# Performance work log

Hardware: AMD Instinct MI355X
Metric: run time of the kernel (lower is better)

Reference implementation:

```python
import jax, jax.numpy as jnp
import numpy as np

N = 20000   # nodes
E = 320000  # edges
F0 = 32     # num_features
H = 8       # GAT heads
G = 64      # graphs in batch


def setup_inputs() -> dict:
    key = jax.random.key(0)
    ks = jax.random.split(key, 16)
    def p(k, shape, s=0.05):
        return jax.random.normal(k, shape, jnp.float32) * s
    d = {}
    d['x'] = jax.random.normal(ks[0], (N, F0), jnp.float32)
    d['edge_index'] = jax.random.randint(ks[1], (2, E), 0, N, dtype=jnp.int32)
    d['edge_weights'] = jax.random.uniform(ks[2], (E,), jnp.float32)
    d['batch'] = jnp.sort(jax.random.randint(ks[3], (N,), 0, G, dtype=jnp.int32))
    # GATConv(32 -> 32, heads=8)
    d['W_gat'] = p(ks[4], (F0, H * F0)); d['att_src'] = p(ks[5], (H, F0))
    d['att_dst'] = p(ks[6], (H, F0));    d['b_gat'] = jnp.zeros((H * F0,), jnp.float32)
    # residual Linear(256 -> 1024) (widened so the residual add is shape-consistent)
    d['W_res'] = p(ks[7], (H * F0, 1024)); d['b_res'] = jnp.zeros((1024,), jnp.float32)
    # GCNConv(256 -> 512) + BN1
    d['W2'] = p(ks[8], (H * F0, 512)); d['b2'] = jnp.zeros((512,), jnp.float32)
    d['g1'] = jnp.ones((512,), jnp.float32); d['be1'] = jnp.zeros((512,), jnp.float32)
    d['m1'] = jnp.zeros((512,), jnp.float32); d['v1'] = jnp.ones((512,), jnp.float32)
    # GCNConv(512 -> 1024) + BN2
    d['W3'] = p(ks[9], (512, 1024)); d['b3'] = jnp.zeros((1024,), jnp.float32)
    d['g2'] = jnp.ones((1024,), jnp.float32); d['be2'] = jnp.zeros((1024,), jnp.float32)
    d['m2'] = jnp.zeros((1024,), jnp.float32); d['v2'] = jnp.ones((1024,), jnp.float32)
    # head
    d['Wf1'] = p(ks[10], (1024, 256)); d['bf1'] = jnp.zeros((256,), jnp.float32)
    d['Wf2'] = p(ks[11], (256, 2));    d['bf2'] = jnp.zeros((2,), jnp.float32)
    return d


def _add_self_loops(edge_index, edge_weight, n):
    loop = jnp.arange(n, dtype=edge_index.dtype)
    ei = jnp.concatenate([edge_index, jnp.stack([loop, loop])], axis=1)
    ew = jnp.concatenate([edge_weight, jnp.ones((n,), edge_weight.dtype)])
    return ei, ew


def _gat(x, edge_index, W, att_src, att_dst, b, n):
    # PyG GATConv, concat=True, eval (attention dropout off). Self-loops already added.
    src, dst = edge_index[0], edge_index[1]
    h = (x @ W).reshape(n, H, -1)                    # [N,H,C]
    a_s = jnp.einsum('nhc,hc->nh', h, att_src)        # [N,H]
    a_d = jnp.einsum('nhc,hc->nh', h, att_dst)
    e = jax.nn.leaky_relu(a_s[src] + a_d[dst], 0.2)   # [E,H]
    m = jax.ops.segment_max(e, dst, num_segments=n)   # softmax over incoming edges
    ex = jnp.exp(e - m[dst])
    s = jax.ops.segment_sum(ex, dst, num_segments=n)
    alpha = ex / s[dst]
    out = jax.ops.segment_sum(h[src] * alpha[:, :, None], dst, num_segments=n)
    return out.reshape(n, -1) + b                     # [N,H*C]


def _gcn(x, edge_index, w, W, b, n):
    # PyG GCNConv with symmetric normalization; self-loops (weight 1) already added.
    src, dst = edge_index[0], edge_index[1]
    deg = jax.ops.segment_sum(w, dst, num_segments=n)
    dinv = jnp.where(deg > 0, jax.lax.rsqrt(jnp.maximum(deg, 1e-12)), 0.0)
    norm = dinv[src] * w * dinv[dst]                  # [E]
    h = x @ W                                         # transform first (cheaper)
    return jax.ops.segment_sum(h[src] * norm[:, None], dst, num_segments=n) + b


def _bn(x, g, b, m, v):
    return g * (x - m) * jax.lax.rsqrt(v + 1e-5) + b


def reference(x, edge_index, edge_weights, batch, W_gat, att_src, att_dst, b_gat,
              W_res, b_res, W2, b2, g1, be1, m1, v1, W3, b3, g2, be2, m2, v2,
              Wf1, bf1, Wf2, bf2):
    n = x.shape[0]
    ei, ew = _add_self_loops(edge_index, edge_weights, n)
    h = jax.nn.relu(_gat(x, ei, W_gat, att_src, att_dst, b_gat, n))   # [N,256]
    res = h @ W_res + b_res                                           # [N,1024]
    h = _gcn(h, ei, ew, W2, b2, n)                                    # [N,512]
    h = jax.nn.relu(_bn(h, g1, be1, m1, v1))
    h = _gcn(h, ei, ew, W3, b3, n)                                    # [N,1024]
    h = jax.nn.relu(_bn(h, g2, be2, m2, v2))
    h = h + res
    pooled = jax.ops.segment_max(h, batch, num_segments=G)            # global max pool [G,1024]
    z = jax.nn.relu(pooled @ Wf1 + bf1)                               # dropout is eval no-op
    return z @ Wf2 + bf2                                              # [G,2]
```

## Files before the change

### kernel.cpp

```cpp
#include <hip/hip_runtime.h>
#include <hip/hip_bf16.h>

#define NN 20000
#define EE 320000
#define GG 64
#define EN (EE + NN)
#define MT 157

typedef float f32x4 __attribute__((ext_vector_type(4)));
typedef __bf16 bf16x4 __attribute__((ext_vector_type(4)));
typedef __bf16 bf16x8 __attribute__((ext_vector_type(8)));

__device__ __forceinline__ void gl_lds16(const void* g, void* l) {
    __builtin_amdgcn_global_load_lds((const __attribute__((address_space(1))) void*)g,
                                     (__attribute__((address_space(3))) void*)l, 16, 0, 0);
}

__global__ void sentinel_kernel(float* out, int n) {
    int i = blockIdx.x * 256 + threadIdx.x;
    if (i < n) out[i] = 12345.0f;
}

__global__ void init_kernel(int* deg_cnt, float* deg_w, int* fill, float* pooled) {
    int i = blockIdx.x * 256 + threadIdx.x;
    if (i < NN) { deg_cnt[i] = 1; deg_w[i] = 1.0f; fill[i] = 0; }
    if (i < GG * 1024) pooled[i] = -INFINITY;
}

__global__ void convert_wt(const float* __restrict__ W, __bf16* __restrict__ Wt, int K, int N) {
    int n = blockIdx.x;
    for (int k = threadIdx.x; k < K; k += 256)
        Wt[(size_t)n * K + k] = (__bf16)W[(size_t)k * N + n];
}

__global__ __launch_bounds__(256) void gat_transform(
    const float* __restrict__ x, const float* __restrict__ W,
    const float* __restrict__ att_s, const float* __restrict__ att_d,
    __bf16* __restrict__ hlin, float* __restrict__ a_s, float* __restrict__ a_d)
{
    __shared__ float Ws[32 * 256];
    int tid = threadIdx.x;
#pragma unroll
    for (int k = 0; k < 32; k++) Ws[k * 256 + tid] = W[k * 256 + tid];
    float asc = att_s[tid], adc = att_d[tid];
    __syncthreads();
    for (int n = blockIdx.x; n < NN; n += gridDim.x) {
        const float* xp = x + (size_t)n * 32;
        float acc = 0.f;
#pragma unroll
        for (int k = 0; k < 32; k++) acc += xp[k] * Ws[k * 256 + tid];
        hlin[(size_t)n * 256 + tid] = (__bf16)acc;
        float s = acc * asc, d = acc * adc;
#pragma unroll
        for (int m = 1; m <= 16; m <<= 1) { s += __shfl_xor(s, m); d += __shfl_xor(d, m); }
        if ((tid & 31) == 0) { int h = tid >> 5; a_s[n * 8 + h] = s; a_d[n * 8 + h] = d; }
    }
}

__global__ void deg_kernel(const int* __restrict__ ei, const float* __restrict__ ew,
                           int* deg_cnt, float* deg_w) {
    int e = blockIdx.x * 256 + threadIdx.x;
    if (e >= EE) return;
    int dst = ei[EE + e];
    atomicAdd(&deg_cnt[dst], 1);
    atomicAdd(&deg_w[dst], ew[e]);
}

__global__ __launch_bounds__(256) void scan_kernel(const int* __restrict__ deg_cnt, int* __restrict__ rowptr) {
    __shared__ int partial[256];
    int tid = threadIdx.x;
    const int chunk = (NN + 255) / 256;
    int s0 = tid * chunk, s1 = min(s0 + chunk, NN);
    int sum = 0;
    for (int i = s0; i < s1; i++) sum += deg_cnt[i];
    partial[tid] = sum;
    __syncthreads();
    if (tid == 0) {
        int run = 0;
        for (int i = 0; i < 256; i++) { int t = partial[i]; partial[i] = run; run += t; }
        rowptr[NN] = run;
    }
    __syncthreads();
    int run = partial[tid];
    for (int i = s0; i < s1; i++) { rowptr[i] = run; run += deg_cnt[i]; }
}

__global__ void fill_kernel(const int* __restrict__ ei, const float* __restrict__ ew,
                            const float* __restrict__ deg_w, const int* __restrict__ rowptr,
                            int* fill, int* __restrict__ csr_src, float* __restrict__ csr_norm) {
    int e = blockIdx.x * 256 + threadIdx.x;
    if (e >= EN) return;
    int src, dst; float w;
    if (e < EE) { src = ei[e]; dst = ei[EE + e]; w = ew[e]; }
    else        { src = dst = e - EE; w = 1.0f; }
    int pos = atomicAdd(&fill[dst], 1);
    int slot = rowptr[dst] + pos;
    csr_src[slot] = src;
    csr_norm[slot] = rsqrtf(deg_w[src]) * w * rsqrtf(deg_w[dst]);
}

__global__ __launch_bounds__(256) void gat_agg(
    const int* __restrict__ rowptr, const int* __restrict__ csr_src,
    const float* __restrict__ a_s, const float* __restrict__ a_d,
    const __bf16* __restrict__ hlin, const float* __restrict__ b_gat,
    __bf16* __restrict__ h1)
{
    int widx = threadIdx.x >> 6, lane = threadIdx.x & 63;
    int node = blockIdx.x * 4 + widx;
    int base = rowptr[node], deg = rowptr[node + 1] - base;
    int hA = lane & 7;
    int eslot = lane >> 3;
    int hB = lane >> 3;
    float adA = a_d[node * 8 + hA];
    float acc[4] = {0.f, 0.f, 0.f, 0.f};

    if (deg <= 64) {
        int sv = (lane < deg) ? csr_src[base + lane] : 0;
        float ev[8];
        float psum = 0.f;
#pragma unroll
        for (int j = 0; j < 8; j++) {
            int e = j * 8 + eslot;
            float v = 0.f;
            if (e < deg) {
                int src = __shfl(sv, e);
                float t = a_s[src * 8 + hA] + adA;
                t = (t > 0.f) ? t : 0.2f * t;
                v = __expf(t);
            }
            ev[j] = v;
            psum += v;
        }
#pragma unroll
        for (int m = 8; m <= 32; m <<= 1) psum += __shfl_xor(psum, m);
        float sinv = 1.f / __shfl(psum, hB);
#pragma unroll
        for (int j = 0; j < 8; j++) {
            if (j * 8 >= deg) break;
            int lim = min(8, deg - j * 8);
            for (int t = 0; t < lim; t++) {
                int s = j * 8 + t;
                int src = __shfl(sv, s);
                float alpha = __shfl(ev[j], (t << 3) | hB) * sinv;
                bf16x4 f = *(const bf16x4*)(hlin + (size_t)src * 256 + lane * 4);
#pragma unroll
                for (int c = 0; c < 4; c++) acc[c] += alpha * (float)f[c];
            }
        }
    } else {
        float sum = 0.f;
        for (int e = 0; e < deg; e++) {
            int src = csr_src[base + e];
            float t = a_s[src * 8 + hA] + adA;
            t = (t > 0.f) ? t : 0.2f * t;
            sum += __expf(t);
        }
        float sinv = 1.f / __shfl(sum, hB);
        float adB = a_d[node * 8 + hB];
        for (int e = 0; e < deg; e++) {
            int src = csr_src[base + e];
            float t = a_s[src * 8 + hB] + adB;
            t = (t > 0.f) ? t : 0.2f * t;
            float alpha = __expf(t) * sinv;
            bf16x4 f = *(const bf16x4*)(hlin + (size_t)src * 256 + lane * 4);
#pragma unroll
            for (int c = 0; c < 4; c++) acc[c] += alpha * (float)f[c];
        }
    }
    float4 bg = *(const float4*)(b_gat + lane * 4);
    bf16x4 o;
    o[0] = (__bf16)fmaxf(acc[0] + bg.x, 0.f);
    o[1] = (__bf16)fmaxf(acc[1] + bg.y, 0.f);
    o[2] = (__bf16)fmaxf(acc[2] + bg.z, 0.f);
    o[3] = (__bf16)fmaxf(acc[3] + bg.w, 0.f);
    *(bf16x4*)(h1 + (size_t)node * 256 + lane * 4) = o;
}

template <int C>
__global__ __launch_bounds__(256) void gcn_agg(
    const int* __restrict__ rowptr, const int* __restrict__ csr_src,
    const float* __restrict__ csr_norm, const __bf16* __restrict__ feat,
    __bf16* __restrict__ out)
{
    constexpr int V = C / 64;
    int widx = threadIdx.x >> 6, lane = threadIdx.x & 63;
    int node = blockIdx.x * 4 + widx;
    int base = rowptr[node], deg = rowptr[node + 1] - base;
    float acc[V];
#pragma unroll
    for (int j = 0; j < V; j++) acc[j] = 0.f;
    const __bf16* fb = feat + lane * V;
    for (int e0 = 0; e0 < deg; e0 += 64) {
        int cnt = min(64, deg - e0);
        int sv = 0; float wv = 0.f;
        if (lane < cnt) { sv = csr_src[base + e0 + lane]; wv = csr_norm[base + e0 + lane]; }
#pragma unroll 4
        for (int s = 0; s < cnt; s++) {
            int src = __shfl(sv, s);
            float w = __shfl(wv, s);
            if constexpr (V == 8) {
                bf16x8 f = *(const bf16x8*)(fb + (size_t)src * C);
#pragma unroll
                for (int j = 0; j < 8; j++) acc[j] += w * (float)f[j];
            } else {
                bf16x4 f = *(const bf16x4*)(fb + (size_t)src * C);
#pragma unroll
                for (int j = 0; j < 4; j++) acc[j] += w * (float)f[j];
            }
        }
    }
    if constexpr (V == 8) {
        bf16x8 o;
#pragma unroll
        for (int j = 0; j < 8; j++) o[j] = (__bf16)acc[j];
        *(bf16x8*)(out + (size_t)node * C + lane * V) = o;
    } else {
        bf16x4 o;
#pragma unroll
        for (int j = 0; j < 4; j++) o[j] = (__bf16)acc[j];
        *(bf16x4*)(out + (size_t)node * C + lane * V) = o;
    }
}


__device__ __forceinline__ void stage_async(
    const __bf16* __restrict__ A, int K, const __bf16* __restrict__ Wt,
    int bm, int bn, int k0, int tid, __bf16* As, __bf16* Bs)
{
#pragma unroll
    for (int i = 0; i < 2; i++) {
        int j = i * 256 + tid;
        int r = j >> 2, c = j & 3;
        const __bf16* gp = A + (size_t)(bm + r) * K + k0 + c * 8;
        gl_lds16(gp, As + (size_t)(j & ~63) * 8);
    }
#pragma unroll
    for (int i = 0; i < 2; i++) {
        int j = i * 256 + tid;
        int r = j >> 2, c = j & 3;
        const __bf16* gp = Wt + (size_t)(bn + r) * K + k0 + c * 8;
        gl_lds16(gp, Bs + (size_t)(j & ~63) * 8);
    }
}

__device__ __forceinline__ void mfma_step(
    const __bf16* As, const __bf16* Bs, int wr, int wc, int l16, int q, f32x4 (&acc)[4][4])
{
    bf16x8 af[4], bfv[4];
#pragma unroll
    for (int mt = 0; mt < 4; mt++) af[mt]  = *(const bf16x8*)(As + (wr * 64 + mt * 16 + l16) * 32 + q * 8);
#pragma unroll
    for (int nt = 0; nt < 4; nt++) bfv[nt] = *(const bf16x8*)(Bs + (wc * 64 + nt * 16 + l16) * 32 + q * 8);
#pragma unroll
    for (int mt = 0; mt < 4; mt++)
#pragma unroll
        for (int nt = 0; nt < 4; nt++)
            acc[mt][nt] = __builtin_amdgcn_mfma_f32_16x16x32_bf16(af[mt], bfv[nt], acc[mt][nt], 0, 0, 0);
}

__device__ __forceinline__ void gemm_loop(
    const __bf16* __restrict__ A, int K, const __bf16* __restrict__ Wt,
    int bm, int bn, int tid, int wr, int wc, int l16, int q,
    __bf16* As, __bf16* Bs, f32x4 (&acc)[4][4])
{
    for (int k0 = 0; k0 < K; k0 += 32) {
        stage_async(A, K, Wt, bm, bn, k0, tid, As, Bs);
        __syncthreads();
        mfma_step(As, Bs, wr, wc, l16, q, acc);
        __syncthreads();
    }
}

__global__ __launch_bounds__(256) void gemm_bn_relu(
    const __bf16* __restrict__ A, const __bf16* __restrict__ Wt,
    int M, int K, int Nc,
    const float* __restrict__ bias,
    const float* __restrict__ g, const float* __restrict__ be,
    const float* __restrict__ mu, const float* __restrict__ var,
    __bf16* __restrict__ C)
{
    __shared__ __bf16 As[128 * 32];
    __shared__ __bf16 Bs[128 * 32];
    int tid = threadIdx.x;
    int w = tid >> 6, wr = w >> 1, wc = w & 1;
    int l = tid & 63, q = l >> 4, l16 = l & 15;
    int i = blockIdx.x;
    int k = (i & 3) * MT + (i >> 2);
    int bm = (k >> 2) * 128, bn = (k & 3) * 128;
    f32x4 acc[4][4] = {};
    gemm_loop(A, K, Wt, bm, bn, tid, wr, wc, l16, q, As, Bs, acc);
#pragma unroll
    for (int nt = 0; nt < 4; nt++) {
        int gn = bn + wc * 64 + nt * 16 + l16;
        float s = g[gn] * rsqrtf(var[gn] + 1e-5f);
        float t = be[gn] - mu[gn] * s;
        float bv = bias[gn];
#pragma unroll
        for (int mt = 0; mt < 4; mt++)
#pragma unroll
            for (int r = 0; r < 4; r++) {
                int gm = bm + wr * 64 + mt * 16 + q * 4 + r;
                if (gm < M) C[(size_t)gm * Nc + gn] = (__bf16)fmaxf((acc[mt][nt][r] + bv) * s + t, 0.f);
            }
    }
}

__device__ __forceinline__ void atomicMaxFloat(float* addr, float value) {
    if (value >= 0.f) atomicMax((int*)addr, __float_as_int(value));
    else              atomicMin((unsigned int*)addr, __float_as_uint(value));
}

__global__ __launch_bounds__(256) void gemm_final(
    const __bf16* __restrict__ A1, const __bf16* __restrict__ W3t,
    const __bf16* __restrict__ A2, const __bf16* __restrict__ Wrt,
    const float* __restrict__ b3, const float* __restrict__ bres,
    const float* __restrict__ g, const float* __restrict__ be,
    const float* __restrict__ mu, const float* __restrict__ var,
    const int* __restrict__ batch, float* __restrict__ pooled)
{
    const int M = NN;
    __shared__ __bf16 As[128 * 32];
    __shared__ __bf16 Bs[128 * 32];
    __shared__ int bat[128];
    int tid = threadIdx.x;
    int w = tid >> 6, wr = w >> 1, wc = w & 1;
    int l = tid & 63, q = l >> 4, l16 = l & 15;
    int i = blockIdx.x;
    int k = (i & 7) * MT + (i >> 3);
    int bm = (k >> 3) * 128, bn = (k & 7) * 128;
    if (tid < 128) bat[tid] = (bm + tid < M) ? batch[bm + tid] : -1;
    f32x4 acc[4][4] = {};
    f32x4 accR[4][4] = {};
    gemm_loop(A1, 512, W3t, bm, bn, tid, wr, wc, l16, q, As, Bs, acc);
    gemm_loop(A2, 256, Wrt, bm, bn, tid, wr, wc, l16, q, As, Bs, accR);
#pragma unroll
    for (int nt = 0; nt < 4; nt++) {
        int gn = bn + wc * 64 + nt * 16 + l16;
        float s = g[gn] * rsqrtf(var[gn] + 1e-5f);
        float t = be[gn] - mu[gn] * s;
        float bv3 = b3[gn];
        float bvr = bres[gn];
        int cb = -1; float run = 0.f;
#pragma unroll
        for (int mt = 0; mt < 4; mt++)
#pragma unroll
            for (int r = 0; r < 4; r++) {
                int lr = wr * 64 + mt * 16 + q * 4 + r;
                int id = bat[lr];
                if (id < 0) continue;
                float v = fmaxf((acc[mt][nt][r] + bv3) * s + t, 0.f) + accR[mt][nt][r] + bvr;
                if (id == cb) run = fmaxf(run, v);
                else {
                    if (cb >= 0) atomicMaxFloat(&pooled[cb * 1024 + gn], run);
                    cb = id; run = v;
                }
            }
        if (cb >= 0) atomicMaxFloat(&pooled[cb * 1024 + gn], run);
    }
}

__global__ __launch_bounds__(256) void head_kernel(
    const float* __restrict__ pooled, const float* __restrict__ Wf1, const float* __restrict__ bf1,
    const float* __restrict__ Wf2, const float* __restrict__ bf2, float* __restrict__ out)
{
    int gph = blockIdx.x, tid = threadIdx.x;
    __shared__ float prow[1024];
    __shared__ float zred[256];
    for (int i = tid; i < 1024; i += 256) prow[i] = pooled[gph * 1024 + i];
    __syncthreads();
    float z = 0.f;
    for (int k = 0; k < 1024; k++) z += prow[k] * Wf1[k * 256 + tid];
    z = fmaxf(z + bf1[tid], 0.f);
    for (int c = 0; c < 2; c++) {
        zred[tid] = z * Wf2[tid * 2 + c];
        __syncthreads();
        for (int s = 128; s > 0; s >>= 1) { if (tid < s) zred[tid] += zred[tid + s]; __syncthreads(); }
        if (tid == 0) out[gph * 2 + c] = zred[0] + bf2[c];
        __syncthreads();
    }
}

extern "C" void kernel_launch(void* const* d_in, const int* in_sizes, int n_in,
                              void* d_out, int out_size, void* d_ws, size_t ws_size,
                              hipStream_t stream) {
    const float* x       = (const float*)d_in[0];
    const int*   ei      = (const int*)d_in[1];
    const float* ew      = (const float*)d_in[2];
    const int*   batch   = (const int*)d_in[3];
    const float* W_gat   = (const float*)d_in[4];
    const float* att_src = (const float*)d_in[5];
    const float* att_dst = (const float*)d_in[6];
    const float* b_gat   = (const float*)d_in[7];
    const float* W_res   = (const float*)d_in[8];
    const float* b_res   = (const float*)d_in[9];
    const float* W2      = (const float*)d_in[10];
    const float* b2v     = (const float*)d_in[11];
    const float* g1      = (const float*)d_in[12];
    const float* be1     = (const float*)d_in[13];
    const float* m1      = (const float*)d_in[14];
    const float* v1      = (const float*)d_in[15];
    const float* W3      = (const float*)d_in[16];
    const float* b3      = (const float*)d_in[17];
    const float* g2      = (const float*)d_in[18];
    const float* be2     = (const float*)d_in[19];
    const float* m2      = (const float*)d_in[20];
    const float* v2      = (const float*)d_in[21];
    const float* Wf1     = (const float*)d_in[22];
    const float* bf1     = (const float*)d_in[23];
    const float* Wf2     = (const float*)d_in[24];
    const float* bf2v    = (const float*)d_in[25];
    float* out           = (float*)d_out;

    char* ws = (char*)d_ws;
    size_t off = 0;
    auto alloc = [&](size_t bytes) { size_t o = off; off += (bytes + 255) & ~(size_t)255; return o; };
    size_t o_hlin   = alloc((size_t)NN * 256 * 2);
    size_t o_h1     = alloc((size_t)NN * 256 * 2);
    size_t o_h2     = alloc((size_t)NN * 512 * 2);
    size_t o_agg2   = alloc((size_t)NN * 512 * 2);
    size_t o_as     = alloc((size_t)NN * 8 * 4);
    size_t o_ad     = alloc((size_t)NN * 8 * 4);
    size_t o_degc   = alloc((size_t)NN * 4);
    size_t o_degw   = alloc((size_t)NN * 4);
    size_t o_rowptr = alloc((size_t)(NN + 1) * 4);
    size_t o_fill   = alloc((size_t)NN * 4);
    size_t o_csrs   = alloc((size_t)EN * 4);
    size_t o_csrn   = alloc((size_t)EN * 4);
    size_t o_pool   = alloc((size_t)GG * 1024 * 4);
    size_t o_w2t    = alloc((size_t)512 * 256 * 2);
    size_t o_w3t    = alloc((size_t)1024 * 512 * 2);
    size_t o_wrt    = alloc((size_t)1024 * 256 * 2);
    if (off > ws_size) {
        sentinel_kernel<<<(out_size + 255) / 256, 256, 0, stream>>>(out, out_size);
        return;
    }

    __bf16* hlin   = (__bf16*)(ws + o_hlin);
    __bf16* agg1   = hlin;
    __bf16* h1     = (__bf16*)(ws + o_h1);
    __bf16* h2     = (__bf16*)(ws + o_h2);
    __bf16* agg2   = (__bf16*)(ws + o_agg2);
    float*  a_s    = (float*)(ws + o_as);
    float*  a_d    = (float*)(ws + o_ad);
    int*    degc   = (int*)(ws + o_degc);
    float*  degw   = (float*)(ws + o_degw);
    int*    rowptr = (int*)(ws + o_rowptr);
    int*    fillb  = (int*)(ws + o_fill);
    int*    csrs   = (int*)(ws + o_csrs);
    float*  csrn   = (float*)(ws + o_csrn);
    float*  pooled = (float*)(ws + o_pool);
    __bf16* W2t    = (__bf16*)(ws + o_w2t);
    __bf16* W3t    = (__bf16*)(ws + o_w3t);
    __bf16* Wrt    = (__bf16*)(ws + o_wrt);

    init_kernel<<<256, 256, 0, stream>>>(degc, degw, fillb, pooled);
    convert_wt<<<512, 256, 0, stream>>>(W2, W2t, 256, 512);
    convert_wt<<<1024, 256, 0, stream>>>(W3, W3t, 512, 1024);
    convert_wt<<<1024, 256, 0, stream>>>(W_res, Wrt, 256, 1024);

    gat_transform<<<512, 256, 0, stream>>>(x, W_gat, att_src, att_dst, hlin, a_s, a_d);
    deg_kernel<<<(EE + 255) / 256, 256, 0, stream>>>(ei, ew, degc, degw);
    scan_kernel<<<1, 256, 0, stream>>>(degc, rowptr);
    fill_kernel<<<(EN + 255) / 256, 256, 0, stream>>>(ei, ew, degw, rowptr, fillb, csrs, csrn);
    gat_agg<<<NN / 4, 256, 0, stream>>>(rowptr, csrs, a_s, a_d, hlin, b_gat, h1);

    gcn_agg<256><<<NN / 4, 256, 0, stream>>>(rowptr, csrs, csrn, h1, agg1);
    gemm_bn_relu<<<4 * MT, 256, 0, stream>>>(agg1, W2t, NN, 256, 512, b2v,
        g1, be1, m1, v1, h2);
    gcn_agg<512><<<NN / 4, 256, 0, stream>>>(rowptr, csrs, csrn, h2, agg2);
    gemm_final<<<8 * MT, 256, 0, stream>>>(agg2, W3t, h1, Wrt,
        b3, b_res, g2, be2, m2, v2, batch, pooled);

    head_kernel<<<GG, 256, 0, stream>>>(pooled, Wf1, bf1, Wf2, bf2v, out);
}
```

Baseline: 465.3 us.

## Double-buffer GEMM LDS staging and split aggregation accumulators for ILP

The GEMM main loop now uses two LDS buffers. The next K-slice is issued asynchronously while MFMAs run on the current one, and one barrier per step replaces two. The GAT and GCN gather loops process two edges per iteration into separate accumulators, so more independent loads are in flight. LDS use per block doubles, which may lower occupancy, and the extra accumulators raise register pressure.

Result: faster. 447.1 us (-3.9%).

```diff
diff --git a/kernel.cpp b/kernel.cpp
--- a/kernel.cpp
+++ b/kernel.cpp
@@ -112,7 +112,8 @@
     int eslot = lane >> 3;
     int hB = lane >> 3;
     float adA = a_d[node * 8 + hA];
-    float acc[4] = {0.f, 0.f, 0.f, 0.f};
+    float acc0[4] = {0.f, 0.f, 0.f, 0.f};
+    float acc1[4] = {0.f, 0.f, 0.f, 0.f};
 
     if (deg <= 64) {
         int sv = (lane < deg) ? csr_src[base + lane] : 0;
@@ -138,13 +139,24 @@
         for (int j = 0; j < 8; j++) {
             if (j * 8 >= deg) break;
             int lim = min(8, deg - j * 8);
-            for (int t = 0; t < lim; t++) {
-                int s = j * 8 + t;
-                int src = __shfl(sv, s);
+            int t = 0;
+            for (; t + 1 < lim; t += 2) {
+                int s0 = j * 8 + t, s1 = s0 + 1;
+                int srcA = __shfl(sv, s0), srcB = __shfl(sv, s1);
+                float aA = __shfl(ev[j], (t << 3) | hB) * sinv;
+                float aB = __shfl(ev[j], ((t + 1) << 3) | hB) * sinv;
+                bf16x4 fA = *(const bf16x4*)(hlin + (size_t)srcA * 256 + lane * 4);
+                bf16x4 fB = *(const bf16x4*)(hlin + (size_t)srcB * 256 + lane * 4);
+#pragma unroll
+                for (int c = 0; c < 4; c++) { acc0[c] += aA * (float)fA[c]; acc1[c] += aB * (float)fB[c]; }
+            }
+            if (t < lim) {
+                int s0 = j * 8 + t;
+                int src = __shfl(sv, s0);
                 float alpha = __shfl(ev[j], (t << 3) | hB) * sinv;
                 bf16x4 f = *(const bf16x4*)(hlin + (size_t)src * 256 + lane * 4);
 #pragma unroll
-                for (int c = 0; c < 4; c++) acc[c] += alpha * (float)f[c];
+                for (int c = 0; c < 4; c++) acc0[c] += alpha * (float)f[c];
             }
         }
     } else {
@@ -164,15 +176,15 @@
             float alpha = __expf(t) * sinv;
             bf16x4 f = *(const bf16x4*)(hlin + (size_t)src * 256 + lane * 4);
 #pragma unroll
-            for (int c = 0; c < 4; c++) acc[c] += alpha * (float)f[c];
+            for (int c = 0; c < 4; c++) acc0[c] += alpha * (float)f[c];
         }
     }
     float4 bg = *(const float4*)(b_gat + lane * 4);
     bf16x4 o;
-    o[0] = (__bf16)fmaxf(acc[0] + bg.x, 0.f);
-    o[1] = (__bf16)fmaxf(acc[1] + bg.y, 0.f);
-    o[2] = (__bf16)fmaxf(acc[2] + bg.z, 0.f);
-    o[3] = (__bf16)fmaxf(acc[3] + bg.w, 0.f);
+    o[0] = (__bf16)fmaxf(acc0[0] + acc1[0] + bg.x, 0.f);
+    o[1] = (__bf16)fmaxf(acc0[1] + acc1[1] + bg.y, 0.f);
+    o[2] = (__bf16)fmaxf(acc0[2] + acc1[2] + bg.z, 0.f);
+    o[3] = (__bf16)fmaxf(acc0[3] + acc1[3] + bg.w, 0.f);
     *(bf16x4*)(h1 + (size_t)node * 256 + lane * 4) = o;
 }
 
@@ -186,38 +198,54 @@
     int widx = threadIdx.x >> 6, lane = threadIdx.x & 63;
     int node = blockIdx.x * 4 + widx;
     int base = rowptr[node], deg = rowptr[node + 1] - base;
-    float acc[V];
-#pragma unroll
-    for (int j = 0; j < V; j++) acc[j] = 0.f;
+    float acc0[V], acc1[V];
+#pragma unroll
+    for (int j = 0; j < V; j++) { acc0[j] = 0.f; acc1[j] = 0.f; }
     const __bf16* fb = feat + lane * V;
     for (int e0 = 0; e0 < deg; e0 += 64) {
         int cnt = min(64, deg - e0);
         int sv = 0; float wv = 0.f;
         if (lane < cnt) { sv = csr_src[base + e0 + lane]; wv = csr_norm[base + e0 + lane]; }
-#pragma unroll 4
-        for (int s = 0; s < cnt; s++) {
+        int s = 0;
+#pragma unroll 2
+        for (; s + 1 < cnt; s += 2) {
+            int srcA = __shfl(sv, s),    srcB = __shfl(sv, s + 1);
+            float wA = __shfl(wv, s),    wB   = __shfl(wv, s + 1);
+            if constexpr (V == 8) {
+                bf16x8 fA = *(const bf16x8*)(fb + (size_t)srcA * C);
+                bf16x8 fB = *(const bf16x8*)(fb + (size_t)srcB * C);
+#pragma unroll
+                for (int j = 0; j < 8; j++) { acc0[j] += wA * (float)fA[j]; acc1[j] += wB * (float)fB[j]; }
+            } else {
+                bf16x4 fA = *(const bf16x4*)(fb + (size_t)srcA * C);
+                bf16x4 fB = *(const bf16x4*)(fb + (size_t)srcB * C);
+#pragma unroll
+                for (int j = 0; j < 4; j++) { acc0[j] += wA * (float)fA[j]; acc1[j] += wB * (float)fB[j]; }
+            }
+        }
+        if (s < cnt) {
             int src = __shfl(sv, s);
             float w = __shfl(wv, s);
             if constexpr (V == 8) {
                 bf16x8 f = *(const bf16x8*)(fb + (size_t)src * C);
 #pragma unroll
-                for (int j = 0; j < 8; j++) acc[j] += w * (float)f[j];
+                for (int j = 0; j < 8; j++) acc0[j] += w * (float)f[j];
             } else {
                 bf16x4 f = *(const bf16x4*)(fb + (size_t)src * C);
 #pragma unroll
-                for (int j = 0; j < 4; j++) acc[j] += w * (float)f[j];
+                for (int j = 0; j < 4; j++) acc0[j] += w * (float)f[j];
             }
         }
     }
     if constexpr (V == 8) {
         bf16x8 o;
 #pragma unroll
-        for (int j = 0; j < 8; j++) o[j] = (__bf16)acc[j];
+        for (int j = 0; j < 8; j++) o[j] = (__bf16)(acc0[j] + acc1[j]);
         *(bf16x8*)(out + (size_t)node * C + lane * V) = o;
     } else {
         bf16x4 o;
 #pragma unroll
-        for (int j = 0; j < 4; j++) o[j] = (__bf16)acc[j];
+        for (int j = 0; j < 4; j++) o[j] = (__bf16)(acc0[j] + acc1[j]);
         *(bf16x4*)(out + (size_t)node * C + lane * V) = o;
     }
 }
@@ -258,17 +286,22 @@
             acc[mt][nt] = __builtin_amdgcn_mfma_f32_16x16x32_bf16(af[mt], bfv[nt], acc[mt][nt], 0, 0, 0);
 }
 
-__device__ __forceinline__ void gemm_loop(
+__device__ __forceinline__ void gemm_loop_db(
     const __bf16* __restrict__ A, int K, const __bf16* __restrict__ Wt,
     int bm, int bn, int tid, int wr, int wc, int l16, int q,
-    __bf16* As, __bf16* Bs, f32x4 (&acc)[4][4])
-{
-    for (int k0 = 0; k0 < K; k0 += 32) {
-        stage_async(A, K, Wt, bm, bn, k0, tid, As, Bs);
+    __bf16* As0, __bf16* Bs0, __bf16* As1, __bf16* Bs1, f32x4 (&acc)[4][4])
+{
+    int nsteps = K >> 5;
+    stage_async(A, K, Wt, bm, bn, 0, tid, As0, Bs0);
+    for (int s = 0; s < nsteps; s++) {
+        __bf16* cA = (s & 1) ? As1 : As0;
+        __bf16* cB = (s & 1) ? Bs1 : Bs0;
         __syncthreads();
-        mfma_step(As, Bs, wr, wc, l16, q, acc);
-        __syncthreads();
-    }
+        if (s + 1 < nsteps)
+            stage_async(A, K, Wt, bm, bn, (s + 1) << 5, tid, (s & 1) ? As0 : As1, (s & 1) ? Bs0 : Bs1);
+        mfma_step(cA, cB, wr, wc, l16, q, acc);
+    }
+    __syncthreads();
 }
 
 __global__ __launch_bounds__(256) void gemm_bn_relu(
@@ -279,8 +312,7 @@
     const float* __restrict__ mu, const float* __restrict__ var,
     __bf16* __restrict__ C)
 {
-    __shared__ __bf16 As[128 * 32];
-    __shared__ __bf16 Bs[128 * 32];
+    __shared__ __bf16 As0[128 * 32], Bs0[128 * 32], As1[128 * 32], Bs1[128 * 32];
     int tid = threadIdx.x;
     int w = tid >> 6, wr = w >> 1, wc = w & 1;
     int l = tid & 63, q = l >> 4, l16 = l & 15;
@@ -288,7 +320,7 @@
     int k = (i & 3) * MT + (i >> 2);
     int bm = (k >> 2) * 128, bn = (k & 3) * 128;
     f32x4 acc[4][4] = {};
-    gemm_loop(A, K, Wt, bm, bn, tid, wr, wc, l16, q, As, Bs, acc);
+    gemm_loop_db(A, K, Wt, bm, bn, tid, wr, wc, l16, q, As0, Bs0, As1, Bs1, acc);
 #pragma unroll
     for (int nt = 0; nt < 4; nt++) {
         int gn = bn + wc * 64 + nt * 16 + l16;
@@ -319,8 +351,7 @@
     const int* __restrict__ batch, float* __restrict__ pooled)
 {
     const int M = NN;
-    __shared__ __bf16 As[128 * 32];
-    __shared__ __bf16 Bs[128 * 32];
+    __shared__ __bf16 As0[128 * 32], Bs0[128 * 32], As1[128 * 32], Bs1[128 * 32];
     __shared__ int bat[128];
     int tid = threadIdx.x;
     int w = tid >> 6, wr = w >> 1, wc = w & 1;
@@ -331,8 +362,8 @@
     if (tid < 128) bat[tid] = (bm + tid < M) ? batch[bm + tid] : -1;
     f32x4 acc[4][4] = {};
     f32x4 accR[4][4] = {};
-    gemm_loop(A1, 512, W3t, bm, bn, tid, wr, wc, l16, q, As, Bs, acc);
-    gemm_loop(A2, 256, Wrt, bm, bn, tid, wr, wc, l16, q, As, Bs, accR);
+    gemm_loop_db(A1, 512, W3t, bm, bn, tid, wr, wc, l16, q, As0, Bs0, As1, Bs1, acc);
+    gemm_loop_db(A2, 256, Wrt, bm, bn, tid, wr, wc, l16, q, As0, Bs0, As1, Bs1, accR);
 #pragma unroll
     for (int nt = 0; nt < 4; nt++) {
         int gn = bn + wc * 64 + nt * 16 + l16;
```

## Tile weight transpose through LDS and unroll gathers with independent accumulators

Applied to the files above, without the earlier changes.

Weight conversion now transposes 64x64 tiles through padded shared memory, so both the reads and the writes are coalesced instead of strided. The GAT and GCN aggregation loops now handle four edges per iteration, issuing four independent row gathers and accumulating into four separate register sets. This aims to raise memory-level parallelism on the random neighbour loads. It costs more registers, which may lower occupancy, and it changes the order of the floating-point summation.

New measurement: 453.7 us. 1.03x faster.

```diff
diff --git a/kernel.cpp b/kernel.cpp
--- a/kernel.cpp
+++ b/kernel.cpp
@@ -27,10 +27,18 @@
     if (i < GG * 1024) pooled[i] = -INFINITY;
 }
 
-__global__ void convert_wt(const float* __restrict__ W, __bf16* __restrict__ Wt, int K, int N) {
-    int n = blockIdx.x;
-    for (int k = threadIdx.x; k < K; k += 256)
-        Wt[(size_t)n * K + k] = (__bf16)W[(size_t)k * N + n];
+__global__ __launch_bounds__(256) void convert_wt(const float* __restrict__ W, __bf16* __restrict__ Wt,
+                                                  int K, int N) {
+    __shared__ float tile[64][65];
+    int kb = blockIdx.y * 64, nb = blockIdx.x * 64;
+    int tx = threadIdx.x & 63, ty = threadIdx.x >> 6;
+#pragma unroll
+    for (int i = ty; i < 64; i += 4)
+        tile[i][tx] = W[(size_t)(kb + i) * N + nb + tx];
+    __syncthreads();
+#pragma unroll
+    for (int i = ty; i < 64; i += 4)
+        Wt[(size_t)(nb + i) * K + kb + tx] = (__bf16)tile[tx][i];
 }
 
 __global__ __launch_bounds__(256) void gat_transform(
@@ -112,7 +120,7 @@
     int eslot = lane >> 3;
     int hB = lane >> 3;
     float adA = a_d[node * 8 + hA];
-    float acc[4] = {0.f, 0.f, 0.f, 0.f};
+    float acc0[4] = {}, acc1[4] = {}, acc2[4] = {}, acc3[4] = {};
 
     if (deg <= 64) {
         int sv = (lane < deg) ? csr_src[base + lane] : 0;
@@ -138,13 +146,30 @@
         for (int j = 0; j < 8; j++) {
             if (j * 8 >= deg) break;
             int lim = min(8, deg - j * 8);
-            for (int t = 0; t < lim; t++) {
-                int s = j * 8 + t;
-                int src = __shfl(sv, s);
+            int t = 0;
+            for (; t + 3 < lim; t += 4) {
+                int sA = __shfl(sv, j * 8 + t),     sB = __shfl(sv, j * 8 + t + 1);
+                int sC = __shfl(sv, j * 8 + t + 2), sD = __shfl(sv, j * 8 + t + 3);
+                float aA = __shfl(ev[j], (t << 3) | hB) * sinv;
+                float aB = __shfl(ev[j], ((t + 1) << 3) | hB) * sinv;
+                float aC = __shfl(ev[j], ((t + 2) << 3) | hB) * sinv;
+                float aD = __shfl(ev[j], ((t + 3) << 3) | hB) * sinv;
+                bf16x4 fA = *(const bf16x4*)(hlin + (size_t)sA * 256 + lane * 4);
+                bf16x4 fB = *(const bf16x4*)(hlin + (size_t)sB * 256 + lane * 4);
+                bf16x4 fC = *(const bf16x4*)(hlin + (size_t)sC * 256 + lane * 4);
+                bf16x4 fD = *(const bf16x4*)(hlin + (size_t)sD * 256 + lane * 4);
+#pragma unroll
+                for (int c = 0; c < 4; c++) {
+                    acc0[c] += aA * (float)fA[c]; acc1[c] += aB * (float)fB[c];
+                    acc2[c] += aC * (float)fC[c]; acc3[c] += aD * (float)fD[c];
+                }
+            }
+            for (; t < lim; t++) {
+                int src = __shfl(sv, j * 8 + t);
                 float alpha = __shfl(ev[j], (t << 3) | hB) * sinv;
                 bf16x4 f = *(const bf16x4*)(hlin + (size_t)src * 256 + lane * 4);
 #pragma unroll
-                for (int c = 0; c < 4; c++) acc[c] += alpha * (float)f[c];
+                for (int c = 0; c < 4; c++) acc0[c] += alpha * (float)f[c];
             }
         }
     } else {
@@ -164,15 +189,15 @@
             float alpha = __expf(t) * sinv;
             bf16x4 f = *(const bf16x4*)(hlin + (size_t)src * 256 + lane * 4);
 #pragma unroll
-            for (int c = 0; c < 4; c++) acc[c] += alpha * (float)f[c];
+            for (int c = 0; c < 4; c++) acc0[c] += alpha * (float)f[c];
         }
     }
     float4 bg = *(const float4*)(b_gat + lane * 4);
     bf16x4 o;
-    o[0] = (__bf16)fmaxf(acc[0] + bg.x, 0.f);
-    o[1] = (__bf16)fmaxf(acc[1] + bg.y, 0.f);
-    o[2] = (__bf16)fmaxf(acc[2] + bg.z, 0.f);
-    o[3] = (__bf16)fmaxf(acc[3] + bg.w, 0.f);
+    o[0] = (__bf16)fmaxf(acc0[0] + acc1[0] + acc2[0] + acc3[0] + bg.x, 0.f);
+    o[1] = (__bf16)fmaxf(acc0[1] + acc1[1] + acc2[1] + acc3[1] + bg.y, 0.f);
+    o[2] = (__bf16)fmaxf(acc0[2] + acc1[2] + acc2[2] + acc3[2] + bg.z, 0.f);
+    o[3] = (__bf16)fmaxf(acc0[3] + acc1[3] + acc2[3] + acc3[3] + bg.w, 0.f);
     *(bf16x4*)(h1 + (size_t)node * 256 + lane * 4) = o;
 }
 
@@ -186,40 +211,43 @@
     int widx = threadIdx.x >> 6, lane = threadIdx.x & 63;
     int node = blockIdx.x * 4 + widx;
     int base = rowptr[node], deg = rowptr[node + 1] - base;
-    float acc[V];
-#pragma unroll
-    for (int j = 0; j < V; j++) acc[j] = 0.f;
+    float acc0[V], acc1[V], acc2[V], acc3[V];
+#pragma unroll
+    for (int j = 0; j < V; j++) { acc0[j] = 0.f; acc1[j] = 0.f; acc2[j] = 0.f; acc3[j] = 0.f; }
     const __bf16* fb = feat + lane * V;
+    typedef __bf16 bf16v __attribute__((ext_vector_type(V)));
     for (int e0 = 0; e0 < deg; e0 += 64) {
         int cnt = min(64, deg - e0);
         int sv = 0; float wv = 0.f;
         if (lane < cnt) { sv = csr_src[base + e0 + lane]; wv = csr_norm[base + e0 + lane]; }
-#pragma unroll 4
-        for (int s = 0; s < cnt; s++) {
+        int s = 0;
+        for (; s + 3 < cnt; s += 4) {
+            int sA = __shfl(sv, s),     sB = __shfl(sv, s + 1);
+            int sC = __shfl(sv, s + 2), sD = __shfl(sv, s + 3);
+            float wA = __shfl(wv, s),     wB = __shfl(wv, s + 1);
+            float wC = __shfl(wv, s + 2), wD = __shfl(wv, s + 3);
+            bf16v fA = *(const bf16v*)(fb + (size_t)sA * C);
+            bf16v fB = *(const bf16v*)(fb + (size_t)sB * C);
+            bf16v fC = *(const bf16v*)(fb + (size_t)sC * C);
+            bf16v fD = *(const bf16v*)(fb + (size_t)sD * C);
+#pragma unroll
+            for (int j = 0; j < V; j++) {
+                acc0[j] += wA * (float)fA[j]; acc1[j] += wB * (float)fB[j];
+                acc2[j] += wC * (float)fC[j]; acc3[j] += wD * (float)fD[j];
+            }
+        }
+        for (; s < cnt; s++) {
             int src = __shfl(sv, s);
             float w = __shfl(wv, s);
-            if constexpr (V == 8) {
-                bf16x8 f = *(const bf16x8*)(fb + (size_t)src * C);
-#pragma unroll
-                for (int j = 0; j < 8; j++) acc[j] += w * (float)f[j];
-            } else {
-                bf16x4 f = *(const bf16x4*)(fb + (size_t)src * C);
-#pragma unroll
-                for (int j = 0; j < 4; j++) acc[j] += w * (float)f[j];
-            }
+            bf16v f = *(const bf16v*)(fb + (size_t)src * C);
+#pragma unroll
+            for (int j = 0; j < V; j++) acc0[j] += w * (float)f[j];
         }
     }
-    if constexpr (V == 8) {
-        bf16x8 o;
-#pragma unroll
-        for (int j = 0; j < 8; j++) o[j] = (__bf16)acc[j];
-        *(bf16x8*)(out + (size_t)node * C + lane * V) = o;
-    } else {
-        bf16x4 o;
-#pragma unroll
-        for (int j = 0; j < 4; j++) o[j] = (__bf16)acc[j];
-        *(bf16x4*)(out + (size_t)node * C + lane * V) = o;
-    }
+    bf16v o;
+#pragma unroll
+    for (int j = 0; j < V; j++) o[j] = (__bf16)(acc0[j] + acc1[j] + acc2[j] + acc3[j]);
+    *(bf16v*)(out + (size_t)node * C + lane * V) = o;
 }
 
 
@@ -454,9 +482,9 @@
     __bf16* Wrt    = (__bf16*)(ws + o_wrt);
 
     init_kernel<<<256, 256, 0, stream>>>(degc, degw, fillb, pooled);
-    convert_wt<<<512, 256, 0, stream>>>(W2, W2t, 256, 512);
-    convert_wt<<<1024, 256, 0, stream>>>(W3, W3t, 512, 1024);
-    convert_wt<<<1024, 256, 0, stream>>>(W_res, Wrt, 256, 1024);
+    convert_wt<<<dim3(512 / 64, 256 / 64), 256, 0, stream>>>(W2, W2t, 256, 512);
+    convert_wt<<<dim3(1024 / 64, 512 / 64), 256, 0, stream>>>(W3, W3t, 512, 1024);
+    convert_wt<<<dim3(1024 / 64, 256 / 64), 256, 0, stream>>>(W_res, Wrt, 256, 1024);
 
     gat_transform<<<512, 256, 0, stream>>>(x, W_gat, att_src, att_dst, hlin, a_s, a_d);
     deg_kernel<<<(EE + 255) / 256, 256, 0, stream>>>(ei, ew, degc, degw);
```
